# Kernel optimization log

Hardware: AMD Instinct MI355X
Metric: run time of the kernel (lower is better)

Reference implementation:

```python
import jax, jax.numpy as jnp
import numpy as np
from jax import lax

T_NO = 200   # filter taps
SUB = 64     # sub_no (C_den.shape[0]); hidden subunits = SUB-1 = 63
E_NO = 2000  # excitatory synapses
I_NO = 500   # inhibitory synapses
T_DATA = 50000
COS_NB = 13
EPS = 1e-8


def make_bases(T_no):
    """Raised-cosine bases exactly as in the torch constructor (numpy constants)."""
    scale, shift = 5.0, 1.0
    x = np.arange(T_no, dtype=np.float64)
    raw = scale * np.log(x + shift + EPS)
    cos_basis = np.zeros((COS_NB, T_no), np.float32)
    for i in range(COS_NB):
        phi = 0.5 * np.pi * i
        b = 0.5 * np.cos(raw - phi) + 0.5
        b[(raw < phi - np.pi) | (raw > phi + np.pi)] = 0.0
        cos_basis[i] = b
    # acausal observation basis: [2*13-1, 2*T_no+1]
    xo = np.arange(-T_no, T_no + 1, dtype=np.float64)
    rawo = scale * np.log(np.abs(xo) + shift + EPS)
    obs_basis = np.zeros((COS_NB * 2 - 1, 2 * T_no + 1), np.float32)
    for i in range(COS_NB):
        phi = 0.5 * np.pi * i
        b = 0.5 * np.cos(rawo - phi) + 0.5
        b[(rawo < phi - np.pi) | (rawo > phi + np.pi)] = 0.0
        if i == 0:
            obs_basis[0] = b
        else:
            obs_basis[2 * i - 1, T_no:] = b[T_no:]      # positive lags
            obs_basis[2 * i, :T_no + 1] = b[:T_no + 1]  # negative lags
    return jnp.asarray(cos_basis), jnp.asarray(obs_basis)


def conv1d(x, kern, groups):
    # x: [1, Cin, L], kern: [Cout, Cin/groups, K] -> [1, Cout, L-K+1]
    return lax.conv_general_dilated(
        x, kern, window_strides=(1,), padding='VALID',
        dimension_numbers=('NCH', 'OIH', 'NCH'), feature_group_count=groups)


def setup_inputs() -> dict:
    key = jax.random.key(0)
    ks = jax.random.split(key, 9)
    return {
        'S_e': jax.random.uniform(ks[0], (T_DATA, E_NO), jnp.float32),
        'S_i': jax.random.uniform(ks[1], (T_DATA, I_NO), jnp.float32),
        'Z_obs': jax.random.normal(ks[2], (T_DATA,), jnp.float32),
        'temp': jnp.float32(0.5),
        'u': jax.random.uniform(ks[3], (T_DATA, SUB - 1, 2), jnp.float32),
        'C_syn_e': jax.random.uniform(ks[4], (SUB, E_NO), jnp.float32),
        'C_syn_i': jax.random.uniform(ks[5], (SUB, I_NO), jnp.float32),
        'W_syn': jax.random.normal(ks[6], (SUB - 1, COS_NB, 2), jnp.float32) * 0.01,
        'W_obs': jax.random.normal(ks[7], (SUB - 1, COS_NB * 2 - 1), jnp.float32) * 0.01,
        'Theta': jax.random.normal(ks[8], (SUB - 1,), jnp.float32) * 0.01,
    }


def reference(S_e, S_i, Z_obs, temp, u, C_syn_e, C_syn_i, W_syn, W_obs, Theta):
    cos_basis, obs_basis = make_bases(T_NO)
    C = W_syn.shape[0]                       # sub_no - 1
    T_data = S_e.shape[0]
    # per-subunit synaptic drive: [T, C]
    syn_e = S_e @ C_syn_e[1:].T
    syn_i = S_i @ C_syn_i[1:].T
    # basis-built causal kernels, flipped as in torch: [C, 1, T_no]
    e_kern = jnp.flip(jnp.einsum('cb,bt->ct', W_syn[:, :, 0], cos_basis), 1)[:, None, :]
    i_kern = jnp.flip(jnp.einsum('cb,bt->ct', W_syn[:, :, 1], cos_basis), 1)[:, None, :]
    # left zero-pad by T_no-1, depthwise grouped conv1d -> [T, C]
    pad_e = jnp.pad(syn_e, ((T_NO - 1, 0), (0, 0))).T[None]  # [1, C, T+T_no-1]
    pad_i = jnp.pad(syn_i, ((T_NO - 1, 0), (0, 0))).T[None]
    filt_e = conv1d(pad_e, e_kern, C)[0].T
    filt_i = conv1d(pad_i, i_kern, C)[0].T
    syn = filt_e + filt_i                    # [T, C]
    # acausal observation filter: 1 -> C channels, kernel 2*T_no+1
    obs_kern = jnp.flip(W_obs @ obs_basis, 1)[:, None, :]    # [C, 1, 2T+1]
    z_pad = jnp.pad(Z_obs, (T_NO, T_NO))[None, None]         # [1, 1, T+2T_no]
    Z_obs_filt = conv1d(z_pad, obs_kern, 1)[0].T             # [T, C]
    # Gumbel-softmax spike sampling over binary logits [L0, 0]
    L0 = syn + Z_obs_filt + Theta                            # [T, C]
    L_hid = jnp.stack([L0, jnp.zeros_like(L0)], axis=2)      # [T, C, 2]
    g = -jnp.log(-jnp.log(u + EPS) + EPS)
    Z_hid = jax.nn.softmax((L_hid + g) / temp, axis=2)[:, :, 0]
    return Z_hid, jax.nn.sigmoid(L0)
```

## Files before the change

### kernel.cpp

```cpp
#include <hip/hip_runtime.h>
#include <math.h>

#define T_NO   200
#define C_NO   63
#define E_NO   2000
#define I_NO   500
#define TD     50000
#define TPAD   50048
#define EPSF   1e-8f

#define WS_HE    0
#define WS_HI    12600
#define WS_HOBS  25200
#define WS_SYNE  50464
#define WS_SYNI  3253536
#define WS_L0T   6456608

#define PADW(w) ((w) + (((w) >> 5) << 2))

__global__ void filters_kernel(const float* __restrict__ Wsyn,
                               const float* __restrict__ Wobs,
                               float* __restrict__ ws) {
    const double PI = 3.14159265358979323846;
    int idx = blockIdx.x * blockDim.x + threadIdx.x;
    int stride = gridDim.x * blockDim.x;

    for (int p = idx; p < 63 * 200; p += stride) {
        int c = p / 200, d = p - c * 200;
        double raw = 5.0 * log((double)d + 1.0 + 1e-8);
        float ae = 0.f, ai = 0.f;
        for (int b = 0; b < 13; ++b) {
            double phi = 0.5 * PI * (double)b;
            float bv = 0.f;
            if (raw >= phi - PI && raw <= phi + PI)
                bv = (float)(0.5 * cos(raw - phi) + 0.5);
            ae += Wsyn[(c * 13 + b) * 2 + 0] * bv;
            ai += Wsyn[(c * 13 + b) * 2 + 1] * bv;
        }
        ws[WS_HE + p] = ae;
        ws[WS_HI + p] = ai;
    }

    for (int p = idx; p < 63 * 401; p += stride) {
        int c = p / 401, d = p - c * 401;
        double raw = 5.0 * log(fabs((double)(d - 200)) + 1.0 + 1e-8);
        float acc = 0.f;
        for (int i = 0; i < 13; ++i) {
            double phi = 0.5 * PI * (double)i;
            float bv = 0.f;
            if (raw >= phi - PI && raw <= phi + PI)
                bv = (float)(0.5 * cos(raw - phi) + 0.5);
            float w;
            if (i == 0) {
                w = Wobs[c * 25];
            } else {
                w = 0.f;
                if (d >= 200) w += Wobs[c * 25 + 2 * i - 1];
                if (d <= 200) w += Wobs[c * 25 + 2 * i];
            }
            acc += w * bv;
        }
        ws[WS_HOBS + p] = acc;
    }
}

__global__ __launch_bounds__(256) void gemm_kernel(const float* __restrict__ S_e,
                                                   const float* __restrict__ S_i,
                                                   const float* __restrict__ Ce,
                                                   const float* __restrict__ Ci,
                                                   float* __restrict__ synE,
                                                   float* __restrict__ synI) {
    __shared__ float As[32 * 68];
    __shared__ float Bs[32 * 68];
    const int bz = blockIdx.z;
    const float* S  = bz ? S_i : S_e;
    const float* Cs = bz ? Ci : Ce;
    float* synT     = bz ? synI : synE;
    const int K     = bz ? I_NO : E_NO;
    int kbeg, kend;
    if (bz == 0) { kbeg = blockIdx.y ? 1000 : 0; kend = kbeg + 1000; }
    else         { kbeg = blockIdx.y ? 256 : 0;  kend = blockIdx.y ? 500 : 256; }

    const int tid = threadIdx.x;
    const int ty = tid >> 4, tx = tid & 15;
    const int t0 = blockIdx.x * 64;

    const int r0 = tid >> 3,          kg0 = (tid & 7) << 2;
    const int r1 = (tid + 256) >> 3,  kg1 = kg0;

    const int nk = (kend - kbeg + 31) / 32;
    float4 pa0, pb0, pa1, pb1;

    auto prefetch = [&](int kc) {
        const int kb = kbeg + kc * 32;
        float4 z = {0.f, 0.f, 0.f, 0.f};
        int k0 = kb + kg0;
        int ta = t0 + r0;
        pa0 = (ta < TD && k0 < kend) ? *(const float4*)(S + (size_t)ta * K + k0) : z;
        pb0 = (r0 < 63 && k0 < kend) ? *(const float4*)(Cs + (size_t)(r0 + 1) * K + k0) : z;
        int tb = t0 + r1;
        pa1 = (tb < TD && k0 < kend) ? *(const float4*)(S + (size_t)tb * K + k0) : z;
        pb1 = (r1 < 63 && k0 < kend) ? *(const float4*)(Cs + (size_t)(r1 + 1) * K + k0) : z;
    };

    float acc[4][4] = {};
    prefetch(0);
    for (int kc = 0; kc < nk; ++kc) {
        __syncthreads();
        As[(kg0 + 0) * 68 + r0] = pa0.x;
        As[(kg0 + 1) * 68 + r0] = pa0.y;
        As[(kg0 + 2) * 68 + r0] = pa0.z;
        As[(kg0 + 3) * 68 + r0] = pa0.w;
        Bs[(kg0 + 0) * 68 + r0] = pb0.x;
        Bs[(kg0 + 1) * 68 + r0] = pb0.y;
        Bs[(kg0 + 2) * 68 + r0] = pb0.z;
        Bs[(kg0 + 3) * 68 + r0] = pb0.w;
        As[(kg1 + 0) * 68 + r1] = pa1.x;
        As[(kg1 + 1) * 68 + r1] = pa1.y;
        As[(kg1 + 2) * 68 + r1] = pa1.z;
        As[(kg1 + 3) * 68 + r1] = pa1.w;
        Bs[(kg1 + 0) * 68 + r1] = pb1.x;
        Bs[(kg1 + 1) * 68 + r1] = pb1.y;
        Bs[(kg1 + 2) * 68 + r1] = pb1.z;
        Bs[(kg1 + 3) * 68 + r1] = pb1.w;
        __syncthreads();
        if (kc + 1 < nk) prefetch(kc + 1);
        #pragma unroll
        for (int kk = 0; kk < 32; ++kk) {
            const float4 a = *(const float4*)&As[kk * 68 + 4 * ty];
            const float4 b = *(const float4*)&Bs[kk * 68 + 4 * tx];
            float av[4] = {a.x, a.y, a.z, a.w};
            float bv[4] = {b.x, b.y, b.z, b.w};
            #pragma unroll
            for (int i = 0; i < 4; ++i)
                #pragma unroll
                for (int j = 0; j < 4; ++j)
                    acc[i][j] += av[i] * bv[j];
        }
    }
    #pragma unroll
    for (int j = 0; j < 4; ++j) {
        int c = 4 * tx + j;
        if (c < 63) {
            #pragma unroll
            for (int i = 0; i < 4; ++i)
                atomicAdd(synT + (size_t)c * TPAD + t0 + 4 * ty + i, acc[i][j]);
        }
    }
}

__device__ inline float4 ldg4(const float* s, int m) {
    return *(const float4*)(s + 4 * m + ((m >> 3) << 2));
}

__global__ __launch_bounds__(256) void fir_kernel(const float* __restrict__ synE,
                                                  const float* __restrict__ synI,
                                                  const float* __restrict__ Z,
                                                  const float* __restrict__ he,
                                                  const float* __restrict__ hi,
                                                  const float* __restrict__ ho,
                                                  const float* __restrict__ Theta,
                                                  float* __restrict__ L0T) {
    __shared__ __align__(16) float sE[1392];
    __shared__ __align__(16) float sI[1392];
    __shared__ __align__(16) float zs[1616];
    __shared__ __align__(16) float heS[200];
    __shared__ __align__(16) float hiS[200];
    __shared__ __align__(16) float hoS[404];

    const int c   = blockIdx.y;
    const int t0  = blockIdx.x * 1024;
    const int tid = threadIdx.x;
    const int base = t0 - 203;

    for (int w = tid; w < 1228; w += 256) {
        int t = base + w;
        bool ok = (t >= 0 && t < TD);
        size_t idx = (size_t)c * TPAD + t;
        sE[PADW(w)] = ok ? synE[idx] : 0.f;
        sI[PADW(w)] = ok ? synI[idx] : 0.f;
    }
    for (int w = tid; w < 1428; w += 256) {
        int t = base + w;
        zs[PADW(w)] = (t >= 0 && t < TD) ? Z[t] : 0.f;
    }
    for (int d = tid; d < 200; d += 256) { heS[d] = he[c * 200 + d]; hiS[d] = hi[c * 200 + d]; }
    for (int d = tid; d < 401; d += 256) hoS[d] = ho[c * 401 + d];
    __syncthreads();

    const float th = Theta[c];
    float acc[4] = {th, th, th, th};

    {
        float4 eLo = ldg4(sE, tid + 50), eHi = ldg4(sE, tid + 51);
        float4 iLo = ldg4(sI, tid + 50), iHi = ldg4(sI, tid + 51);
        for (int dg = 0; dg < 50; ++dg) {
            const float4 h_e = *(const float4*)(heS + 4 * dg);
            const float4 h_i = *(const float4*)(hiS + 4 * dg);
            const float ew[8] = {eLo.x, eLo.y, eLo.z, eLo.w, eHi.x, eHi.y, eHi.z, eHi.w};
            const float iw[8] = {iLo.x, iLo.y, iLo.z, iLo.w, iHi.x, iHi.y, iHi.z, iHi.w};
            const float heq[4] = {h_e.x, h_e.y, h_e.z, h_e.w};
            const float hiq[4] = {h_i.x, h_i.y, h_i.z, h_i.w};
            #pragma unroll
            for (int q = 0; q < 4; ++q)
                #pragma unroll
                for (int r = 0; r < 4; ++r) {
                    const int o = 3 + r - q;
                    acc[r] += ew[o] * heq[q] + iw[o] * hiq[q];
                }
            eHi = eLo; iHi = iLo;
            if (dg < 49) { eLo = ldg4(sE, tid + 49 - dg); iLo = ldg4(sI, tid + 49 - dg); }
        }
    }
    {
        float4 zLo = ldg4(zs, tid + 100), zHi = ldg4(zs, tid + 101);
        for (int dg = 0; dg < 100; ++dg) {
            const float4 h_o = *(const float4*)(hoS + 4 * dg);
            const float zw[8] = {zLo.x, zLo.y, zLo.z, zLo.w, zHi.x, zHi.y, zHi.z, zHi.w};
            const float hoq[4] = {h_o.x, h_o.y, h_o.z, h_o.w};
            #pragma unroll
            for (int q = 0; q < 4; ++q)
                #pragma unroll
                for (int r = 0; r < 4; ++r) {
                    const int o = 3 + r - q;
                    acc[r] += zw[o] * hoq[q];
                }
            zHi = zLo;
            if (dg < 99) zLo = ldg4(zs, tid + 99 - dg);
        }
        const float h400 = hoS[400];
        #pragma unroll
        for (int r = 0; r < 4; ++r) {
            int w = 4 * tid + 3 + r;
            acc[r] += zs[PADW(w)] * h400;
        }
    }

    const int tb = t0 + 4 * tid;
    if (tb + 3 < TD) {
        float4 v = {acc[0], acc[1], acc[2], acc[3]};
        *(float4*)(L0T + (size_t)c * TPAD + tb) = v;
    } else {
        #pragma unroll
        for (int r = 0; r < 4; ++r)
            if (tb + r < TD) L0T[(size_t)c * TPAD + tb + r] = acc[r];
    }
}

__global__ __launch_bounds__(256) void out_kernel(const float* __restrict__ L0T,
                                                  const float* __restrict__ u,
                                                  const float* __restrict__ temp_p,
                                                  float* __restrict__ out) {
    __shared__ float tile[63 * 65];
    const int t0 = blockIdx.x * 64;
    const int tid = threadIdx.x;

    for (int l = tid; l < 1008; l += 256) {
        int cc = l >> 4;
        int jg = (l & 15) << 2;
        float4 v = *(const float4*)(L0T + (size_t)cc * TPAD + t0 + jg);
        tile[cc * 65 + jg + 0] = v.x;
        tile[cc * 65 + jg + 1] = v.y;
        tile[cc * 65 + jg + 2] = v.z;
        tile[cc * 65 + jg + 3] = v.w;
    }
    __syncthreads();

    const float inv_temp = 1.f / (*temp_p);
    for (int l = tid; l < 4032; l += 256) {
        int tl = l / 63;
        int cc = l - tl * 63;
        int t = t0 + tl;
        if (t < TD) {
            float L0 = tile[cc * 65 + tl];
            float2 uv = *(const float2*)(u + 2 * ((size_t)t * 63 + cc));
            float g0 = -logf(-logf(uv.x + EPSF) + EPSF);
            float g1 = -logf(-logf(uv.y + EPSF) + EPSF);
            float zh = 1.f / (1.f + expf(-((L0 + g0 - g1) * inv_temp)));
            float sg = 1.f / (1.f + expf(-L0));
            out[(size_t)t * 63 + cc] = zh;
            out[3150000 + (size_t)t * 63 + cc] = sg;
        }
    }
}

extern "C" void kernel_launch(void* const* d_in, const int* in_sizes, int n_in,
                              void* d_out, int out_size, void* d_ws, size_t ws_size,
                              hipStream_t stream) {
    (void)in_sizes; (void)n_in; (void)out_size; (void)ws_size;
    const float* S_e   = (const float*)d_in[0];
    const float* S_i   = (const float*)d_in[1];
    const float* Z     = (const float*)d_in[2];
    const float* temp  = (const float*)d_in[3];
    const float* u     = (const float*)d_in[4];
    const float* Ce    = (const float*)d_in[5];
    const float* Ci    = (const float*)d_in[6];
    const float* Wsyn  = (const float*)d_in[7];
    const float* Wobs  = (const float*)d_in[8];
    const float* Theta = (const float*)d_in[9];
    float* out = (float*)d_out;
    float* ws  = (float*)d_ws;

    float* he   = ws + WS_HE;
    float* hi   = ws + WS_HI;
    float* ho   = ws + WS_HOBS;
    float* synE = ws + WS_SYNE;
    float* synI = ws + WS_SYNI;
    float* L0T  = ws + WS_L0T;

    hipLaunchKernelGGL(filters_kernel, dim3(50), dim3(256), 0, stream, Wsyn, Wobs, ws);
    hipMemsetAsync(synE, 0, (size_t)(2 * 3203072) * sizeof(float), stream);
    hipLaunchKernelGGL(gemm_kernel, dim3(782, 2, 2), dim3(256), 0, stream,
                       S_e, S_i, Ce, Ci, synE, synI);
    hipLaunchKernelGGL(fir_kernel, dim3(49, 63), dim3(256), 0, stream,
                       synE, synI, Z, he, hi, ho, Theta, L0T);
    hipLaunchKernelGGL(out_kernel, dim3(782), dim3(256), 0, stream, L0T, u, temp, out);
}
```

Baseline: 1.041 ms.

## Use bf16 MFMA for synapse GEMM with split-K partial buffers instead of atomics

Replaces the fp32 FMA tiled GEMM with a bf16 MFMA (16x16x32) kernel. The weight matrices are converted to padded bf16 in a prep kernel, and the activations are converted on the fly during the load. Split-K results now go to separate partial buffers that the FIR kernel sums, which removes the memset and the atomicAdds. The basis computation moves to its own kernel with tables precomputed once. Rounding the inputs to bf16 lowers precision, and the FIR kernel reads extra partial buffers.

```diff
diff --git a/kernel.cpp b/kernel.cpp
--- a/kernel.cpp
+++ b/kernel.cpp
@@ -9,152 +9,196 @@
 #define TPAD   50048
 #define EPSF   1e-8f
 
+typedef float f32x4 __attribute__((ext_vector_type(4)));
+typedef short s16x8 __attribute__((ext_vector_type(8)));
+
 #define WS_HE    0
 #define WS_HI    12600
 #define WS_HOBS  25200
-#define WS_SYNE  50464
-#define WS_SYNI  3253536
-#define WS_L0T   6456608
+#define WS_COSB  50464
+#define WS_OBSB  53064
+#define WS_BE    63104
+#define WS_BI    128640
+#define WS_PE0   145024
+#define PBSZ     3203072
+#define WS_PI    9754240
+#define WS_L0T   12957312
 
 #define PADW(w) ((w) + (((w) >> 5) << 2))
 
-__global__ void filters_kernel(const float* __restrict__ Wsyn,
-                               const float* __restrict__ Wobs,
-                               float* __restrict__ ws) {
+__device__ inline unsigned short f2bf(float x) {
+    unsigned u = __float_as_uint(x);
+    return (unsigned short)((u + 0x7FFFu + ((u >> 16) & 1u)) >> 16);
+}
+__device__ inline unsigned pack2(float lo, float hi) {
+    return (unsigned)f2bf(lo) | ((unsigned)f2bf(hi) << 16);
+}
+
+__global__ void basis_kernel(float* __restrict__ ws) {
     const double PI = 3.14159265358979323846;
     int idx = blockIdx.x * blockDim.x + threadIdx.x;
     int stride = gridDim.x * blockDim.x;
-
+    for (int p = idx; p < 13 * 200; p += stride) {
+        int i = p / 200, t = p - i * 200;
+        double raw = 5.0 * log((double)t + 1.0 + 1e-8);
+        double phi = 0.5 * PI * (double)i;
+        float b = (raw >= phi - PI && raw <= phi + PI) ? (float)(0.5 * cos(raw - phi) + 0.5) : 0.f;
+        ws[WS_COSB + p] = b;
+    }
+    for (int p = idx; p < 25 * 401; p += stride) {
+        int j = p / 401, x = p - j * 401;
+        int i = (j + 1) >> 1;
+        double raw = 5.0 * log(fabs((double)(x - 200)) + 1.0 + 1e-8);
+        double phi = 0.5 * PI * (double)i;
+        float b = (raw >= phi - PI && raw <= phi + PI) ? (float)(0.5 * cos(raw - phi) + 0.5) : 0.f;
+        if (j > 0) {
+            if (j & 1) { if (x < 200) b = 0.f; }
+            else       { if (x > 200) b = 0.f; }
+        }
+        ws[WS_OBSB + p] = b;
+    }
+}
+
+__global__ void prep_kernel(const float* __restrict__ Wsyn, const float* __restrict__ Wobs,
+                            const float* __restrict__ Ce, const float* __restrict__ Ci,
+                            float* __restrict__ ws) {
+    int idx = blockIdx.x * blockDim.x + threadIdx.x;
+    int stride = gridDim.x * blockDim.x;
     for (int p = idx; p < 63 * 200; p += stride) {
-        int c = p / 200, d = p - c * 200;
-        double raw = 5.0 * log((double)d + 1.0 + 1e-8);
+        int c = p / 200, t = p - c * 200;
         float ae = 0.f, ai = 0.f;
+        #pragma unroll
         for (int b = 0; b < 13; ++b) {
-            double phi = 0.5 * PI * (double)b;
-            float bv = 0.f;
-            if (raw >= phi - PI && raw <= phi + PI)
-                bv = (float)(0.5 * cos(raw - phi) + 0.5);
+            float bv = ws[WS_COSB + b * 200 + t];
             ae += Wsyn[(c * 13 + b) * 2 + 0] * bv;
             ai += Wsyn[(c * 13 + b) * 2 + 1] * bv;
         }
         ws[WS_HE + p] = ae;
         ws[WS_HI + p] = ai;
     }
-
     for (int p = idx; p < 63 * 401; p += stride) {
-        int c = p / 401, d = p - c * 401;
-        double raw = 5.0 * log(fabs((double)(d - 200)) + 1.0 + 1e-8);
-        float acc = 0.f;
-        for (int i = 0; i < 13; ++i) {
-            double phi = 0.5 * PI * (double)i;
-            float bv = 0.f;
-            if (raw >= phi - PI && raw <= phi + PI)
-                bv = (float)(0.5 * cos(raw - phi) + 0.5);
-            float w;
-            if (i == 0) {
-                w = Wobs[c * 25];
-            } else {
-                w = 0.f;
-                if (d >= 200) w += Wobs[c * 25 + 2 * i - 1];
-                if (d <= 200) w += Wobs[c * 25 + 2 * i];
-            }
-            acc += w * bv;
-        }
-        ws[WS_HOBS + p] = acc;
-    }
-}
-
-__global__ __launch_bounds__(256) void gemm_kernel(const float* __restrict__ S_e,
-                                                   const float* __restrict__ S_i,
-                                                   const float* __restrict__ Ce,
-                                                   const float* __restrict__ Ci,
-                                                   float* __restrict__ synE,
-                                                   float* __restrict__ synI) {
-    __shared__ float As[32 * 68];
-    __shared__ float Bs[32 * 68];
-    const int bz = blockIdx.z;
-    const float* S  = bz ? S_i : S_e;
-    const float* Cs = bz ? Ci : Ce;
-    float* synT     = bz ? synI : synE;
-    const int K     = bz ? I_NO : E_NO;
-    int kbeg, kend;
-    if (bz == 0) { kbeg = blockIdx.y ? 1000 : 0; kend = kbeg + 1000; }
-    else         { kbeg = blockIdx.y ? 256 : 0;  kend = blockIdx.y ? 500 : 256; }
-
-    const int tid = threadIdx.x;
-    const int ty = tid >> 4, tx = tid & 15;
-    const int t0 = blockIdx.x * 64;
-
-    const int r0 = tid >> 3,          kg0 = (tid & 7) << 2;
-    const int r1 = (tid + 256) >> 3,  kg1 = kg0;
-
-    const int nk = (kend - kbeg + 31) / 32;
-    float4 pa0, pb0, pa1, pb1;
-
-    auto prefetch = [&](int kc) {
-        const int kb = kbeg + kc * 32;
-        float4 z = {0.f, 0.f, 0.f, 0.f};
-        int k0 = kb + kg0;
-        int ta = t0 + r0;
-        pa0 = (ta < TD && k0 < kend) ? *(const float4*)(S + (size_t)ta * K + k0) : z;
-        pb0 = (r0 < 63 && k0 < kend) ? *(const float4*)(Cs + (size_t)(r0 + 1) * K + k0) : z;
-        int tb = t0 + r1;
-        pa1 = (tb < TD && k0 < kend) ? *(const float4*)(S + (size_t)tb * K + k0) : z;
-        pb1 = (r1 < 63 && k0 < kend) ? *(const float4*)(Cs + (size_t)(r1 + 1) * K + k0) : z;
+        int c = p / 401, x = p - c * 401;
+        float a = 0.f;
+        #pragma unroll
+        for (int j = 0; j < 25; ++j)
+            a += Wobs[c * 25 + j] * ws[WS_OBSB + j * 401 + x];
+        ws[WS_HOBS + p] = a;
+    }
+    unsigned short* Be = (unsigned short*)(ws + WS_BE);
+    for (int p = idx; p < 64 * 2048; p += stride) {
+        int c = p >> 11, k = p & 2047;
+        float v = (c < 63 && k < E_NO) ? Ce[(size_t)(c + 1) * E_NO + k] : 0.f;
+        Be[p] = f2bf(v);
+    }
+    unsigned short* Bi = (unsigned short*)(ws + WS_BI);
+    for (int p = idx; p < 64 * 512; p += stride) {
+        int c = p >> 9, k = p & 511;
+        float v = (c < 63 && k < I_NO) ? Ci[(size_t)(c + 1) * I_NO + k] : 0.f;
+        Bi[p] = f2bf(v);
+    }
+}
+
+#define LDA 40
+__global__ __launch_bounds__(128, 4) void gemm_kernel(const float* __restrict__ S_e,
+                                                      const float* __restrict__ S_i,
+                                                      float* __restrict__ ws) {
+    __shared__ unsigned int Asu[128 * 20];
+    __shared__ unsigned int Bsu[64 * 20];
+
+    const int y = blockIdx.y;
+    const bool isE = (y < 3);
+    const float* S = isE ? S_e : S_i;
+    const unsigned short* Bm = (const unsigned short*)(ws + (isE ? WS_BE : WS_BI));
+    const int K     = isE ? E_NO : I_NO;
+    const int Kpad  = isE ? 2048 : 512;
+    const int kb    = isE ? y * 672 : 0;
+    const int nst   = isE ? 21 : 16;
+    float* outp = ws + (isE ? (WS_PE0 + (size_t)y * PBSZ) : WS_PI);
+
+    const int tid  = threadIdx.x;
+    const int lane = tid & 63;
+    const int w    = tid >> 6;
+    const int t0   = blockIdx.x * 128;
+
+    const int tA = t0 + tid;
+    const float* Srow = S + (size_t)tA * K;
+    const int bc = tid & 63, bseg = tid >> 6;
+
+    unsigned au[16];
+    unsigned pbv[8];
+
+    auto pf = [&](int s) {
+        const int kk = kb + 32 * s;
+        #pragma unroll
+        for (int g = 0; g < 8; ++g) {
+            int k = kk + 4 * g;
+            float4 v = {0.f, 0.f, 0.f, 0.f};
+            if (tA < TD && k < K) v = *(const float4*)(Srow + k);
+            au[2 * g]     = pack2(v.x, v.y);
+            au[2 * g + 1] = pack2(v.z, v.w);
+        }
+        const uint4* bp = (const uint4*)(Bm + (size_t)bc * Kpad + kk + bseg * 16);
+        uint4 b0 = bp[0], b1 = bp[1];
+        pbv[0] = b0.x; pbv[1] = b0.y; pbv[2] = b0.z; pbv[3] = b0.w;
+        pbv[4] = b1.x; pbv[5] = b1.y; pbv[6] = b1.z; pbv[7] = b1.w;
     };
 
-    float acc[4][4] = {};
-    prefetch(0);
-    for (int kc = 0; kc < nk; ++kc) {
+    f32x4 acc[4][4] = {};
+    pf(0);
+    for (int s = 0; s < nst; ++s) {
         __syncthreads();
-        As[(kg0 + 0) * 68 + r0] = pa0.x;
-        As[(kg0 + 1) * 68 + r0] = pa0.y;
-        As[(kg0 + 2) * 68 + r0] = pa0.z;
-        As[(kg0 + 3) * 68 + r0] = pa0.w;
-        Bs[(kg0 + 0) * 68 + r0] = pb0.x;
-        Bs[(kg0 + 1) * 68 + r0] = pb0.y;
-        Bs[(kg0 + 2) * 68 + r0] = pb0.z;
-        Bs[(kg0 + 3) * 68 + r0] = pb0.w;
-        As[(kg1 + 0) * 68 + r1] = pa1.x;
-        As[(kg1 + 1) * 68 + r1] = pa1.y;
-        As[(kg1 + 2) * 68 + r1] = pa1.z;
-        As[(kg1 + 3) * 68 + r1] = pa1.w;
-        Bs[(kg1 + 0) * 68 + r1] = pb1.x;
-        Bs[(kg1 + 1) * 68 + r1] = pb1.y;
-        Bs[(kg1 + 2) * 68 + r1] = pb1.z;
-        Bs[(kg1 + 3) * 68 + r1] = pb1.w;
+        uint4* ap = (uint4*)(Asu + tid * 20);
+        ap[0] = make_uint4(au[0], au[1], au[2], au[3]);
+        ap[1] = make_uint4(au[4], au[5], au[6], au[7]);
+        ap[2] = make_uint4(au[8], au[9], au[10], au[11]);
+        ap[3] = make_uint4(au[12], au[13], au[14], au[15]);
+        uint4* bp2 = (uint4*)(Bsu + bc * 20 + bseg * 8);
+        bp2[0] = make_uint4(pbv[0], pbv[1], pbv[2], pbv[3]);
+        bp2[1] = make_uint4(pbv[4], pbv[5], pbv[6], pbv[7]);
         __syncthreads();
-        if (kc + 1 < nk) prefetch(kc + 1);
-        #pragma unroll
-        for (int kk = 0; kk < 32; ++kk) {
-            const float4 a = *(const float4*)&As[kk * 68 + 4 * ty];
-            const float4 b = *(const float4*)&Bs[kk * 68 + 4 * tx];
-            float av[4] = {a.x, a.y, a.z, a.w};
-            float bv[4] = {b.x, b.y, b.z, b.w};
+        if (s + 1 < nst) pf(s + 1);
+
+        const unsigned short* As = (const unsigned short*)Asu;
+        const unsigned short* Bs = (const unsigned short*)Bsu;
+        const int klocal = (lane >> 4) * 8;
+        s16x8 af[4], bf[4];
+        #pragma unroll
+        for (int ta = 0; ta < 4; ++ta) {
+            int row = 64 * w + 16 * ta + (lane & 15);
+            af[ta] = *(const s16x8*)(As + row * LDA + klocal);
+        }
+        #pragma unroll
+        for (int cb = 0; cb < 4; ++cb) {
+            int col = 16 * cb + (lane & 15);
+            bf[cb] = *(const s16x8*)(Bs + col * LDA + klocal);
+        }
+        #pragma unroll
+        for (int ta = 0; ta < 4; ++ta)
             #pragma unroll
-            for (int i = 0; i < 4; ++i)
-                #pragma unroll
-                for (int j = 0; j < 4; ++j)
-                    acc[i][j] += av[i] * bv[j];
-        }
-    }
+            for (int cb = 0; cb < 4; ++cb)
+                acc[ta][cb] = __builtin_amdgcn_mfma_f32_16x16x32_bf16(af[ta], bf[cb], acc[ta][cb], 0, 0, 0);
+    }
+
+    const int cl = lane & 15, rq = 4 * (lane >> 4);
     #pragma unroll
-    for (int j = 0; j < 4; ++j) {
-        int c = 4 * tx + j;
-        if (c < 63) {
-            #pragma unroll
-            for (int i = 0; i < 4; ++i)
-                atomicAdd(synT + (size_t)c * TPAD + t0 + 4 * ty + i, acc[i][j]);
-        }
-    }
+    for (int ta = 0; ta < 4; ++ta)
+        #pragma unroll
+        for (int cb = 0; cb < 4; ++cb) {
+            int c = 16 * cb + cl;
+            float* dst = outp + (size_t)c * TPAD + t0 + 64 * w + 16 * ta + rq;
+            f32x4 v = acc[ta][cb];
+            *(float4*)dst = make_float4(v.x, v.y, v.z, v.w);
+        }
 }
 
 __device__ inline float4 ldg4(const float* s, int m) {
     return *(const float4*)(s + 4 * m + ((m >> 3) << 2));
 }
 
-__global__ __launch_bounds__(256) void fir_kernel(const float* __restrict__ synE,
-                                                  const float* __restrict__ synI,
+__global__ __launch_bounds__(256) void fir_kernel(const float* __restrict__ pE0,
+                                                  const float* __restrict__ pE1,
+                                                  const float* __restrict__ pE2,
+                                                  const float* __restrict__ pI0,
                                                   const float* __restrict__ Z,
                                                   const float* __restrict__ he,
                                                   const float* __restrict__ hi,
@@ -177,8 +221,13 @@
         int t = base + w;
         bool ok = (t >= 0 && t < TD);
         size_t idx = (size_t)c * TPAD + t;
-        sE[PADW(w)] = ok ? synE[idx] : 0.f;
-        sI[PADW(w)] = ok ? synI[idx] : 0.f;
+        float ve = 0.f, vi = 0.f;
+        if (ok) {
+            ve = pE0[idx] + pE1[idx] + pE2[idx];
+            vi = pI0[idx];
+        }
+        sE[PADW(w)] = ve;
+        sI[PADW(w)] = vi;
     }
     for (int w = tid; w < 1428; w += 256) {
         int t = base + w;
@@ -301,18 +350,12 @@
     float* out = (float*)d_out;
     float* ws  = (float*)d_ws;
 
-    float* he   = ws + WS_HE;
-    float* hi   = ws + WS_HI;
-    float* ho   = ws + WS_HOBS;
-    float* synE = ws + WS_SYNE;
-    float* synI = ws + WS_SYNI;
-    float* L0T  = ws + WS_L0T;
-
-    hipLaunchKernelGGL(filters_kernel, dim3(50), dim3(256), 0, stream, Wsyn, Wobs, ws);
-    hipMemsetAsync(synE, 0, (size_t)(2 * 3203072) * sizeof(float), stream);
-    hipLaunchKernelGGL(gemm_kernel, dim3(782, 2, 2), dim3(256), 0, stream,
-                       S_e, S_i, Ce, Ci, synE, synI);
+    hipLaunchKernelGGL(basis_kernel, dim3(50), dim3(256), 0, stream, ws);
+    hipLaunchKernelGGL(prep_kernel, dim3(256), dim3(256), 0, stream, Wsyn, Wobs, Ce, Ci, ws);
+    hipLaunchKernelGGL(gemm_kernel, dim3(391, 4), dim3(128), 0, stream, S_e, S_i, ws);
     hipLaunchKernelGGL(fir_kernel, dim3(49, 63), dim3(256), 0, stream,
-                       synE, synI, Z, he, hi, ho, Theta, L0T);
-    hipLaunchKernelGGL(out_kernel, dim3(782), dim3(256), 0, stream, L0T, u, temp, out);
-}
+                       ws + WS_PE0, ws + WS_PE0 + PBSZ, ws + WS_PE0 + 2 * (size_t)PBSZ,
+                       ws + WS_PI, Z,
+                       ws + WS_HE, ws + WS_HI, ws + WS_HOBS, Theta, ws + WS_L0T);
+    hipLaunchKernelGGL(out_kernel, dim3(782), dim3(256), 0, stream, ws + WS_L0T, u, temp, out);
+}
```

Result: no change. 1.021 ms (-1.9%).
